# Optimization experiments

Hardware: AMD Instinct MI355X
Metric: run time of the kernel (lower is better)

## Reference

```python
import jax, jax.numpy as jnp
import numpy as np

N_NODES = 100000


def gcn_conv(x, edge_index, W, b):
    """PyG-style GCNConv: symmetric-normalized A+I propagation of x @ W, plus bias."""
    n = x.shape[0]
    src, dst = edge_index[0], edge_index[1]
    loops = jnp.arange(n, dtype=src.dtype)
    src = jnp.concatenate([src, loops])  # add self loops
    dst = jnp.concatenate([dst, loops])
    deg = jax.ops.segment_sum(jnp.ones_like(src, dtype=x.dtype), dst, num_segments=n)
    dinv = jnp.where(deg > 0, jax.lax.rsqrt(deg), 0.0)
    norm = dinv[src] * dinv[dst]  # [E+n]
    h = x @ W  # [n, out]
    msg = h[src] * norm[:, None]  # gather + scale
    out = jax.ops.segment_sum(msg, dst, num_segments=n)  # scatter-add
    return out + b


def setup_inputs() -> dict:
    key = jax.random.key(0)
    ks = jax.random.split(key, 5)
    x = jax.random.normal(ks[0], (N_NODES, 4), dtype=jnp.float32)
    edge_index = jax.random.randint(ks[1], (2, 3200000), 0, N_NODES, dtype=jnp.int64)
    W1 = jax.random.normal(ks[2], (4, 64), dtype=jnp.float32) * 0.5
    b1 = jnp.zeros((64,), dtype=jnp.float32)
    W2 = jax.random.normal(ks[3], (64, 32), dtype=jnp.float32) * 0.125
    b2 = jnp.zeros((32,), dtype=jnp.float32)
    return {"x": x, "edge_index": edge_index, "W1": W1, "b1": b1, "W2": W2, "b2": b2}


def reference(x, edge_index, W1, b1, W2, b2):
    h = gcn_conv(x, edge_index, W1, b1)
    h = jax.nn.relu(h)
    # F.dropout with training=False is identity (eval-mode reference)
    h = gcn_conv(h, edge_index, W2, b2)
    return jnp.mean(h, axis=0)  # [32]
```

## Files before the change

### kernel.cpp

```cpp
#include <hip/hip_runtime.h>

#define ST 512
#define EPB 6400
#define HT 1024
#define FT 1024
#define S_LOG 8
#define S 256
#define SN 196
#define MAGIC 21913099u
#define CAP 6912
#define MAXB 512

__device__ __forceinline__ void gAtomAdd(float* p, float v) {
    unsafeAtomicAdd(p, v);
}

__device__ __forceinline__ int bkt(int key) {
    return (int)__umulhi((unsigned)key, MAGIC);
}

__global__ void k_init(int* __restrict__ cur_d, int* __restrict__ cur_s,
                       float* __restrict__ g, int nb) {
    int t = threadIdx.x;
    if (t < nb) { cur_d[t] = t * CAP; cur_s[t] = t * CAP; }
    if (t < 64) g[t] = 0.0f;
}

__global__ void __launch_bounds__(ST) k_sctr2(
        const int4* __restrict__ src4, const int4* __restrict__ dst4, int E,
        int* __restrict__ cur_d, int* __restrict__ cur_s,
        unsigned* __restrict__ rec_d, unsigned* __restrict__ rec_s, int nb) {
    __shared__ unsigned lrec[EPB];
    __shared__ unsigned short lbkt[EPB];
    __shared__ int cnt[MAXB];
    __shared__ int lst[MAXB];
    __shared__ int gb[MAXB];
    __shared__ int wsum[8];
    int t = threadIdx.x;
    int lane = t & 63, wv = t >> 6;
    int E4 = E >> 2;
    int m = min(EPB, E - blockIdx.x * EPB);
    int m4 = m >> 2;
    int b4 = blockIdx.x * (EPB / 4);

    int4 dk[4], sk[4];
    bool v[4];
    #pragma unroll
    for (int k = 0; k < 4; ++k) {
        int li = k * ST + t;
        int idx = b4 + li;
        v[k] = (li < m4) && (idx < E4);
        if (v[k]) { dk[k] = dst4[idx]; sk[k] = src4[idx]; }
    }

    for (int ph = 0; ph < 2; ++ph) {
        int* cursor = ph ? cur_s : cur_d;
        unsigned* rec = ph ? rec_s : rec_d;
        cnt[t] = 0;
        __syncthreads();
        int rk[16];
        #pragma unroll
        for (int k = 0; k < 4; ++k) {
            if (v[k]) {
                int4 K = ph ? sk[k] : dk[k];
                rk[4 * k + 0] = atomicAdd(&cnt[bkt(K.x)], 1);
                rk[4 * k + 1] = atomicAdd(&cnt[bkt(K.y)], 1);
                rk[4 * k + 2] = atomicAdd(&cnt[bkt(K.z)], 1);
                rk[4 * k + 3] = atomicAdd(&cnt[bkt(K.w)], 1);
            }
        }
        __syncthreads();
        int c = cnt[t];
        int ic = c;
        #pragma unroll
        for (int o = 1; o < 64; o <<= 1) {
            int u = __shfl_up(ic, o);
            if (lane >= o) ic += u;
        }
        if (lane == 63) wsum[wv] = ic;
        __syncthreads();
        int pre = 0;
        #pragma unroll
        for (int k = 0; k < 7; ++k) pre += (k < wv) ? wsum[k] : 0;
        ic += pre;
        lst[t] = ic - c;
        gb[t] = (c > 0) ? atomicAdd(&cursor[t], c) : 0;
        __syncthreads();
        #pragma unroll
        for (int k = 0; k < 4; ++k) {
            if (v[k]) {
                int4 K = ph ? sk[k] : dk[k];
                int4 P = ph ? dk[k] : sk[k];
                int bb, p;
                bb = bkt(K.x); p = lst[bb] + rk[4 * k + 0];
                lrec[p] = ((unsigned)P.x << S_LOG) | (unsigned)(K.x - bb * SN);
                lbkt[p] = (unsigned short)bb;
                bb = bkt(K.y); p = lst[bb] + rk[4 * k + 1];
                lrec[p] = ((unsigned)P.y << S_LOG) | (unsigned)(K.y - bb * SN);
                lbkt[p] = (unsigned short)bb;
                bb = bkt(K.z); p = lst[bb] + rk[4 * k + 2];
                lrec[p] = ((unsigned)P.z << S_LOG) | (unsigned)(K.z - bb * SN);
                lbkt[p] = (unsigned short)bb;
                bb = bkt(K.w); p = lst[bb] + rk[4 * k + 3];
                lrec[p] = ((unsigned)P.w << S_LOG) | (unsigned)(K.w - bb * SN);
                lbkt[p] = (unsigned short)bb;
            }
        }
        __syncthreads();
        for (int i = t; i < m; i += ST) {
            int bb = lbkt[i];
            rec[gb[bb] + (i - lst[bb])] = lrec[i];
        }
        __syncthreads();
    }
}

__global__ void __launch_bounds__(HT) k_hist(
        const unsigned* __restrict__ rec_d, const int* __restrict__ cur_d,
        const float4* __restrict__ x, float* __restrict__ dinv,
        float4* __restrict__ y, int n) {
    __shared__ int cnt[S];
    int b = blockIdx.x, t = threadIdx.x;
    if (t < S) cnt[t] = 0;
    __syncthreads();
    int lo = b * CAP;
    int m = cur_d[b] - lo;
    int m4 = m >> 2;
    const uint4* rec4 = (const uint4*)(rec_d + lo);
    for (int i = t; i < m4; i += HT) {
        uint4 r = rec4[i];
        atomicAdd(&cnt[r.x & (S - 1)], 1);
        atomicAdd(&cnt[r.y & (S - 1)], 1);
        atomicAdd(&cnt[r.z & (S - 1)], 1);
        atomicAdd(&cnt[r.w & (S - 1)], 1);
    }
    for (int i = (m4 << 2) + t; i < m; i += HT)
        atomicAdd(&cnt[rec_d[lo + i] & (S - 1)], 1);
    __syncthreads();
    int nd = b * SN + t;
    if (t < SN && nd < n) {
        float dv = rsqrtf((float)cnt[t] + 1.0f);
        dinv[nd] = dv;
        float4 xi = x[nd];
        y[nd] = make_float4(dv * xi.x, dv * xi.y, dv * xi.z, dv * xi.w);
    }
}

__global__ void __launch_bounds__(FT) k_fuse(
        const unsigned* __restrict__ rec_d, const unsigned* __restrict__ rec_s,
        const int* __restrict__ cur_d, const int* __restrict__ cur_s,
        const float4* __restrict__ y, const float* __restrict__ dinv,
        const float* __restrict__ W1, const float* __restrict__ b1,
        float* __restrict__ g, int n) {
    __shared__ unsigned lrec[CAP];
    __shared__ int cnt[S];
    __shared__ int nst[S];
    __shared__ float a[S];
    __shared__ float4 lp1[S];
    __shared__ float red[FT];
    __shared__ int wsum[4];
    int b = blockIdx.x, t = threadIdx.x;
    int lane = t & 63, wv = t >> 6;
    if (t < S) { cnt[t] = 0; a[t] = 0.0f; }
    __syncthreads();
    int lo = b * CAP;
    int md = cur_d[b] - lo;
    unsigned rv[7]; int rr[7];
    #pragma unroll
    for (int k = 0; k < 7; ++k) {
        int i = t + k * FT;
        if (i < md) {
            unsigned r = rec_d[lo + i];
            rv[k] = r;
            rr[k] = atomicAdd(&cnt[r & (S - 1)], 1);
        }
    }
    __syncthreads();
    int c = 0, ic = 0;
    if (t < S) {
        c = cnt[t]; ic = c;
        #pragma unroll
        for (int o = 1; o < 64; o <<= 1) {
            int u = __shfl_up(ic, o);
            if (lane >= o) ic += u;
        }
        if (lane == 63) wsum[wv] = ic;
    }
    __syncthreads();
    if (t < S) {
        int pre = 0;
        #pragma unroll
        for (int k = 0; k < 3; ++k) pre += (k < wv) ? wsum[k] : 0;
        ic += pre;
        cnt[t] = ic;
        nst[t] = ic - c;
    }
    __syncthreads();
    #pragma unroll
    for (int k = 0; k < 7; ++k) {
        int i = t + k * FT;
        if (i < md) lrec[nst[rv[k] & (S - 1)] + rr[k]] = rv[k] >> S_LOG;
    }
    int ms = cur_s[b] - lo;
    int ms4 = ms >> 2;
    const uint4* rs4 = (const uint4*)(rec_s + lo);
    for (int i = t; i < ms4; i += FT) {
        uint4 r = rs4[i];
        float d0 = dinv[r.x >> S_LOG], d1 = dinv[r.y >> S_LOG];
        float d2 = dinv[r.z >> S_LOG], d3 = dinv[r.w >> S_LOG];
        atomicAdd(&a[r.x & (S - 1)], d0);
        atomicAdd(&a[r.y & (S - 1)], d1);
        atomicAdd(&a[r.z & (S - 1)], d2);
        atomicAdd(&a[r.w & (S - 1)], d3);
    }
    for (int i = (ms4 << 2) + t; i < ms; i += FT) {
        unsigned r = rec_s[lo + i];
        atomicAdd(&a[r & (S - 1)], dinv[r >> S_LOG]);
    }
    __syncthreads();
    int node = t >> 2, q = t & 3;
    int nd = b * SN + node;
    if (node < SN && nd < n) {
        int j1 = cnt[node];
        int j = nst[node] + q;
        float a0 = 0.0f, a1 = 0.0f, a2 = 0.0f, a3 = 0.0f;
        for (; j + 12 < j1; j += 16) {
            int s0 = lrec[j], s1 = lrec[j + 4], s2 = lrec[j + 8], s3 = lrec[j + 12];
            float4 y0 = y[s0], y1 = y[s1], y2 = y[s2], y3 = y[s3];
            a0 += y0.x + y1.x + y2.x + y3.x;
            a1 += y0.y + y1.y + y2.y + y3.y;
            a2 += y0.z + y1.z + y2.z + y3.z;
            a3 += y0.w + y1.w + y2.w + y3.w;
        }
        for (; j < j1; j += 4) {
            float4 ys = y[lrec[j]];
            a0 += ys.x; a1 += ys.y; a2 += ys.z; a3 += ys.w;
        }
        a0 += __shfl_down(a0, 2); a1 += __shfl_down(a1, 2);
        a2 += __shfl_down(a2, 2); a3 += __shfl_down(a3, 2);
        a0 += __shfl_down(a0, 1); a1 += __shfl_down(a1, 1);
        a2 += __shfl_down(a2, 1); a3 += __shfl_down(a3, 1);
        if (q == 0) {
            float di = dinv[nd];
            lp1[node] = make_float4(di * a0, di * a1, di * a2, di * a3);
        }
    }
    __syncthreads();
    int cch = t & 63, w = t >> 6;
    float w0 = W1[cch], w1 = W1[64 + cch], w2 = W1[128 + cch], w3 = W1[192 + cch];
    float bb = b1[cch];
    int nb0 = b * SN;
    float facc = 0.0f;
    for (int k = w; k < SN; k += 16) {
        int ndk = nb0 + k;
        if (ndk >= n) break;
        float di = dinv[ndk];
        float4 p = lp1[k];
        float4 yi = y[ndk];
        float h0 = fmaf(di, yi.x, p.x);
        float h1 = fmaf(di, yi.y, p.y);
        float h2 = fmaf(di, yi.z, p.z);
        float h3 = fmaf(di, yi.w, p.w);
        float h = fmaf(h0, w0, fmaf(h1, w1, fmaf(h2, w2, fmaf(h3, w3, bb))));
        h = fmaxf(h, 0.0f);
        float wi = fmaf(di, a[k], di * di);
        facc = fmaf(wi, h, facc);
    }
    red[t] = facc;
    __syncthreads();
    if (t < 64) {
        float s = red[t];
        #pragma unroll
        for (int o = 1; o < 16; ++o) s += red[t + 64 * o];
        gAtomAdd(&g[t], s);
    }
}

__global__ void k_final(const float* __restrict__ g, const float* __restrict__ W2,
                        const float* __restrict__ b2, float* __restrict__ out, float inv_n) {
    int j = threadIdx.x;
    if (j < 32) {
        float a = 0.0f;
        #pragma unroll
        for (int c = 0; c < 64; ++c) a = fmaf(g[c], W2[c * 32 + j], a);
        out[j] = fmaf(a, inv_n, b2[j]);
    }
}

extern "C" void kernel_launch(void* const* d_in, const int* in_sizes, int n_in,
                              void* d_out, int out_size, void* d_ws, size_t ws_size,
                              hipStream_t stream) {
    const float* x  = (const float*)d_in[0];
    const int*   ei = (const int*)d_in[1];
    const float* W1 = (const float*)d_in[2];
    const float* b1 = (const float*)d_in[3];
    const float* W2 = (const float*)d_in[4];
    const float* b2 = (const float*)d_in[5];
    float* out = (float*)d_out;

    int n = in_sizes[0] / 4;
    int E = in_sizes[1] / 2;
    const int* src = ei;
    const int* dst = ei + E;
    int NB = (n + SN - 1) / SN;

    char* ws = (char*)d_ws;
    int* cur_d = (int*)ws;
    int* cur_s = cur_d + 512;
    float* g   = (float*)(cur_s + 512);
    size_t ctrl = 1600;
    unsigned* rec_d = (unsigned*)ws + ctrl;
    unsigned* rec_s = rec_d + (size_t)NB * CAP;
    float* y    = (float*)(rec_s + (size_t)NB * CAP);
    float* dinv = y + 4 * (size_t)n;

    int NSB = (E + EPB - 1) / EPB;

    k_init<<<1, 512, 0, stream>>>(cur_d, cur_s, g, NB);
    k_sctr2<<<NSB, ST, 0, stream>>>((const int4*)src, (const int4*)dst, E,
                                    cur_d, cur_s, rec_d, rec_s, NB);
    k_hist<<<NB, HT, 0, stream>>>(rec_d, cur_d, (const float4*)x, dinv,
                                  (float4*)y, n);
    k_fuse<<<NB, FT, 0, stream>>>(rec_d, rec_s, cur_d, cur_s,
                                  (const float4*)y, dinv, W1, b1, g, n);
    k_final<<<1, 64, 0, stream>>>(g, W2, b2, out, 1.0f / (float)n);
}
```

Measured before the change: 153.1 us.

## Halve k_fuse block size and restructure bucket sort to free registers

The fused kernel drops from 1024 to 512 threads per block with a launch-bounds occupancy hint. The dst-record counting is merged with the src-side dinv accumulation into one vectorized pass. Scattering into the local sorted list now re-reads the records and takes atomic slot reservations instead of keeping 7 records per thread in registers. The aim is lower register pressure, higher occupancy and fewer barriers, at the cost of a second global read of rec_d, more shared-memory atomics, and two lanes instead of four per node in the gather.

```diff
diff --git a/kernel.cpp b/kernel.cpp
--- a/kernel.cpp
+++ b/kernel.cpp
@@ -3,7 +3,7 @@
 #define ST 512
 #define EPB 6400
 #define HT 1024
-#define FT 1024
+#define FT 512
 #define S_LOG 8
 #define S 256
 #define SN 196
@@ -146,7 +146,7 @@
     }
 }
 
-__global__ void __launch_bounds__(FT) k_fuse(
+__global__ void __launch_bounds__(FT, 8) k_fuse(
         const unsigned* __restrict__ rec_d, const unsigned* __restrict__ rec_s,
         const int* __restrict__ cur_d, const int* __restrict__ cur_s,
         const float4* __restrict__ y, const float* __restrict__ dinv,
@@ -155,6 +155,7 @@
     __shared__ unsigned lrec[CAP];
     __shared__ int cnt[S];
     __shared__ int nst[S];
+    __shared__ int nc[S];
     __shared__ float a[S];
     __shared__ float4 lp1[S];
     __shared__ float red[FT];
@@ -165,15 +166,34 @@
     __syncthreads();
     int lo = b * CAP;
     int md = cur_d[b] - lo;
-    unsigned rv[7]; int rr[7];
-    #pragma unroll
-    for (int k = 0; k < 7; ++k) {
-        int i = t + k * FT;
-        if (i < md) {
-            unsigned r = rec_d[lo + i];
-            rv[k] = r;
-            rr[k] = atomicAdd(&cnt[r & (S - 1)], 1);
-        }
+    int ms = cur_s[b] - lo;
+    int md4 = md >> 2, ms4 = ms >> 2;
+    const uint4* rd4 = (const uint4*)(rec_d + lo);
+    const uint4* rs4 = (const uint4*)(rec_s + lo);
+    int lim4 = max(md4, ms4);
+    for (int i = t; i < lim4; i += FT) {
+        if (i < md4) {
+            uint4 r = rd4[i];
+            atomicAdd(&cnt[r.x & (S - 1)], 1);
+            atomicAdd(&cnt[r.y & (S - 1)], 1);
+            atomicAdd(&cnt[r.z & (S - 1)], 1);
+            atomicAdd(&cnt[r.w & (S - 1)], 1);
+        }
+        if (i < ms4) {
+            uint4 r = rs4[i];
+            float d0 = dinv[r.x >> S_LOG], d1 = dinv[r.y >> S_LOG];
+            float d2 = dinv[r.z >> S_LOG], d3 = dinv[r.w >> S_LOG];
+            atomicAdd(&a[r.x & (S - 1)], d0);
+            atomicAdd(&a[r.y & (S - 1)], d1);
+            atomicAdd(&a[r.z & (S - 1)], d2);
+            atomicAdd(&a[r.w & (S - 1)], d3);
+        }
+    }
+    for (int i = (md4 << 2) + t; i < md; i += FT)
+        atomicAdd(&cnt[rec_d[lo + i] & (S - 1)], 1);
+    for (int i = (ms4 << 2) + t; i < ms; i += FT) {
+        unsigned r = rec_s[lo + i];
+        atomicAdd(&a[r & (S - 1)], dinv[r >> S_LOG]);
     }
     __syncthreads();
     int c = 0, ic = 0;
@@ -194,50 +214,41 @@
         ic += pre;
         cnt[t] = ic;
         nst[t] = ic - c;
-    }
-    __syncthreads();
-    #pragma unroll
-    for (int k = 0; k < 7; ++k) {
-        int i = t + k * FT;
-        if (i < md) lrec[nst[rv[k] & (S - 1)] + rr[k]] = rv[k] >> S_LOG;
-    }
-    int ms = cur_s[b] - lo;
-    int ms4 = ms >> 2;
-    const uint4* rs4 = (const uint4*)(rec_s + lo);
-    for (int i = t; i < ms4; i += FT) {
-        uint4 r = rs4[i];
-        float d0 = dinv[r.x >> S_LOG], d1 = dinv[r.y >> S_LOG];
-        float d2 = dinv[r.z >> S_LOG], d3 = dinv[r.w >> S_LOG];
-        atomicAdd(&a[r.x & (S - 1)], d0);
-        atomicAdd(&a[r.y & (S - 1)], d1);
-        atomicAdd(&a[r.z & (S - 1)], d2);
-        atomicAdd(&a[r.w & (S - 1)], d3);
-    }
-    for (int i = (ms4 << 2) + t; i < ms; i += FT) {
-        unsigned r = rec_s[lo + i];
-        atomicAdd(&a[r & (S - 1)], dinv[r >> S_LOG]);
-    }
-    __syncthreads();
-    int node = t >> 2, q = t & 3;
+        nc[t]  = ic - c;
+    }
+    __syncthreads();
+    for (int i = t; i < md4; i += FT) {
+        uint4 r = rd4[i];
+        int p;
+        p = atomicAdd(&nc[r.x & (S - 1)], 1); lrec[p] = r.x >> S_LOG;
+        p = atomicAdd(&nc[r.y & (S - 1)], 1); lrec[p] = r.y >> S_LOG;
+        p = atomicAdd(&nc[r.z & (S - 1)], 1); lrec[p] = r.z >> S_LOG;
+        p = atomicAdd(&nc[r.w & (S - 1)], 1); lrec[p] = r.w >> S_LOG;
+    }
+    for (int i = (md4 << 2) + t; i < md; i += FT) {
+        unsigned r = rec_d[lo + i];
+        int p = atomicAdd(&nc[r & (S - 1)], 1);
+        lrec[p] = r >> S_LOG;
+    }
+    __syncthreads();
+    int node = t >> 1, q = t & 1;
     int nd = b * SN + node;
     if (node < SN && nd < n) {
         int j1 = cnt[node];
         int j = nst[node] + q;
         float a0 = 0.0f, a1 = 0.0f, a2 = 0.0f, a3 = 0.0f;
-        for (; j + 12 < j1; j += 16) {
-            int s0 = lrec[j], s1 = lrec[j + 4], s2 = lrec[j + 8], s3 = lrec[j + 12];
+        for (; j + 6 < j1; j += 8) {
+            int s0 = lrec[j], s1 = lrec[j + 2], s2 = lrec[j + 4], s3 = lrec[j + 6];
             float4 y0 = y[s0], y1 = y[s1], y2 = y[s2], y3 = y[s3];
             a0 += y0.x + y1.x + y2.x + y3.x;
             a1 += y0.y + y1.y + y2.y + y3.y;
             a2 += y0.z + y1.z + y2.z + y3.z;
             a3 += y0.w + y1.w + y2.w + y3.w;
         }
-        for (; j < j1; j += 4) {
+        for (; j < j1; j += 2) {
             float4 ys = y[lrec[j]];
             a0 += ys.x; a1 += ys.y; a2 += ys.z; a3 += ys.w;
         }
-        a0 += __shfl_down(a0, 2); a1 += __shfl_down(a1, 2);
-        a2 += __shfl_down(a2, 2); a3 += __shfl_down(a3, 2);
         a0 += __shfl_down(a0, 1); a1 += __shfl_down(a1, 1);
         a2 += __shfl_down(a2, 1); a3 += __shfl_down(a3, 1);
         if (q == 0) {
@@ -251,7 +262,7 @@
     float bb = b1[cch];
     int nb0 = b * SN;
     float facc = 0.0f;
-    for (int k = w; k < SN; k += 16) {
+    for (int k = w; k < SN; k += 8) {
         int ndk = nb0 + k;
         if (ndk >= n) break;
         float di = dinv[ndk];
@@ -271,7 +282,7 @@
     if (t < 64) {
         float s = red[t];
         #pragma unroll
-        for (int o = 1; o < 16; ++o) s += red[t + 64 * o];
+        for (int o = 1; o < 8; ++o) s += red[t + 64 * o];
         gAtomAdd(&g[t], s);
     }
 }
```

After: 160.9 us. +5.1%, slower.
